# Performance work log

Measured on AMD Instinct MI355X. Metric: run time of the kernel, lower is better.

## Reference

```python
import jax, jax.numpy as jnp
import numpy as np

DIM = 1024
HEADS = 8
DIM_HEAD = 64
HIDDEN = HEADS * DIM_HEAD  # 512
SCALE = DIM_HEAD ** -0.5
BATCH = 16384
EPS = 1e-12  # F.normalize eps


def setup_inputs() -> dict:
    key = jax.random.key(0)
    k0, k1, k2 = jax.random.split(key, 3)
    x = jax.random.normal(k0, (BATCH, DIM), dtype=jnp.float32)
    w_qkv = jax.random.normal(k1, (3 * HIDDEN, DIM), dtype=jnp.float32) * 0.02
    w_out = jax.random.normal(k2, (DIM, HIDDEN), dtype=jnp.float32) * 0.02
    b_out = jnp.zeros((DIM,), dtype=jnp.float32)
    g = jnp.ones((1, DIM), dtype=jnp.float32)
    return {"x": x, "w_qkv": w_qkv, "w_out": w_out, "b_out": b_out, "g": g}


def reference(x, w_qkv, w_out, b_out, g):
    b = x.shape[0]
    # Conv1d(kernel=1, no bias) on n=1 sequence == matmul with (3*hidden, dim) weight
    qkv = x @ w_qkv.T  # (b, 3*hidden)
    q, k, v = jnp.split(qkv, 3, axis=1)  # each (b, hidden)
    # rearrange 'b (h c) n -> b h c n' with n=1 -> (b, h, c)
    q = q.reshape(b, HEADS, DIM_HEAD)
    k = k.reshape(b, HEADS, DIM_HEAD)
    v = v.reshape(b, HEADS, DIM_HEAD)
    # q.softmax(dim=-2) is over the c axis
    q = jax.nn.softmax(q, axis=-1) * SCALE
    # k.softmax(dim=-1) is over the n axis of size 1 -> all ones (kept faithful)
    k = jax.nn.softmax(k[..., None], axis=-1)[..., 0]
    # context = einsum('bhdn,bhen->bhde', k, v); out = einsum('bhde,bhdn->bhen', context, q)
    # with n=1 this collapses to out_e = (sum_d k_d q_d) * v_e; fused to avoid (b,h,d,e)
    s = jnp.einsum('bhd,bhd->bh', k, q)  # (b, h)
    out = s[..., None] * v  # (b, h, e)
    out = out.reshape(b, HIDDEN)  # 'b h c n -> b (h c) n', squeeze(-1)
    # Linear(hidden, dim)
    out = out @ w_out.T + b_out  # (b, dim)
    # RMSNorm_MLP: F.normalize(x, dim=1) * g * sqrt(dim)
    norm = jnp.linalg.norm(out, axis=1, keepdims=True)
    out = out / jnp.maximum(norm, EPS) * g * jnp.sqrt(jnp.float32(DIM))
    return out
```

## Files before the change

kernel.cpp:

```cpp
#include <hip/hip_runtime.h>
#include <hip/hip_bf16.h>


typedef __attribute__((ext_vector_type(8))) short bf16x8;
typedef __attribute__((ext_vector_type(4))) float f32x4;

#define BLK 128
#define BK  32

struct alignas(16) bfvec8 { __hip_bfloat16 h[8]; };

__global__ __launch_bounds__(256)
void cast_bf16(const float* __restrict__ in, bfvec8* __restrict__ out, int n8) {
    int i = blockIdx.x * blockDim.x + threadIdx.x;
    if (i >= n8) return;
    const float4* p = (const float4*)in + (size_t)i * 2;
    float4 a = p[0];
    float4 b = p[1];
    bfvec8 o;
    o.h[0] = __float2bfloat16(a.x); o.h[1] = __float2bfloat16(a.y);
    o.h[2] = __float2bfloat16(a.z); o.h[3] = __float2bfloat16(a.w);
    o.h[4] = __float2bfloat16(b.x); o.h[5] = __float2bfloat16(b.y);
    o.h[6] = __float2bfloat16(b.z); o.h[7] = __float2bfloat16(b.w);
    out[i] = o;
}

template<bool WRITE_BF16>
__global__ __launch_bounds__(256)
void gemm_bt(const __hip_bfloat16* __restrict__ A,
             const __hip_bfloat16* __restrict__ Bt,
             void* __restrict__ Cout,
             const float* __restrict__ bias,
             int M, int N, int K, float alpha)
{
    __shared__ __align__(16) __hip_bfloat16 As[BLK * BK];
    __shared__ __align__(16) __hip_bfloat16 Bs[BLK * BK];

    const int tid  = threadIdx.x;
    const int lane = tid & 63;
    const int wave = tid >> 6;
    const int wm   = wave >> 1;
    const int wn   = wave & 1;
    const int quad = lane >> 4;
    const int tr   = lane & 15;

    const int m0 = blockIdx.y * BLK;
    const int n0 = blockIdx.x * BLK;

    f32x4 acc[4][4];
#pragma unroll
    for (int i = 0; i < 4; ++i)
#pragma unroll
        for (int j = 0; j < 4; ++j)
            acc[i][j] = (f32x4){0.f, 0.f, 0.f, 0.f};

    for (int kt = 0; kt < K; kt += BK) {
#pragma unroll
        for (int i = 0; i < 2; ++i) {
            int L  = i * 256 + wave * 64 + lane;
            int r  = L >> 2;
            int c8 = (L & 3) << 3;
            const __hip_bfloat16* ga = A  + (size_t)(m0 + r) * K + kt + c8;
            const __hip_bfloat16* gb = Bt + (size_t)(n0 + r) * K + kt + c8;
            __builtin_amdgcn_global_load_lds(
                (const __attribute__((address_space(1))) void*)ga,
                (__attribute__((address_space(3))) void*)(As + (size_t)L * 8), 16, 0, 0);
            __builtin_amdgcn_global_load_lds(
                (const __attribute__((address_space(1))) void*)gb,
                (__attribute__((address_space(3))) void*)(Bs + (size_t)L * 8), 16, 0, 0);
        }
        __syncthreads();

        bf16x8 af[4], bf[4];
#pragma unroll
        for (int mi = 0; mi < 4; ++mi)
            af[mi] = *(const bf16x8*)(As + ((wm * 64 + mi * 16 + tr) * BK + quad * 8));
#pragma unroll
        for (int ni = 0; ni < 4; ++ni)
            bf[ni] = *(const bf16x8*)(Bs + ((wn * 64 + ni * 16 + tr) * BK + quad * 8));

#pragma unroll
        for (int mi = 0; mi < 4; ++mi)
#pragma unroll
            for (int ni = 0; ni < 4; ++ni)
                acc[mi][ni] = __builtin_amdgcn_mfma_f32_16x16x32_bf16(
                    af[mi], bf[ni], acc[mi][ni], 0, 0, 0);

        __syncthreads();
    }

#pragma unroll
    for (int mi = 0; mi < 4; ++mi) {
#pragma unroll
        for (int ni = 0; ni < 4; ++ni) {
            const int col = n0 + wn * 64 + ni * 16 + tr;
            float b = 0.f;
            if (!WRITE_BF16 && bias != nullptr) b = bias[col];
#pragma unroll
            for (int r = 0; r < 4; ++r) {
                const int row = m0 + wm * 64 + mi * 16 + quad * 4 + r;
                float val = acc[mi][ni][r] * alpha + b;
                if (WRITE_BF16)
                    ((__hip_bfloat16*)Cout)[(size_t)row * N + col] = __float2bfloat16(val);
                else
                    ((float*)Cout)[(size_t)row * N + col] = val;
            }
        }
    }
}

__global__ __launch_bounds__(256)
void rmsnorm_rows(float* __restrict__ y, const float* __restrict__ g) {
    const int row = blockIdx.x;
    const int tid = threadIdx.x;
    float* p = y + (size_t)row * 1024 + tid * 4;
    float4 v = *(float4*)p;
    float ss = v.x * v.x + v.y * v.y + v.z * v.z + v.w * v.w;
#pragma unroll
    for (int off = 32; off > 0; off >>= 1)
        ss += __shfl_down(ss, off, 64);
    __shared__ float wsum[4];
    if ((tid & 63) == 0) wsum[tid >> 6] = ss;
    __syncthreads();
    const float total = wsum[0] + wsum[1] + wsum[2] + wsum[3];
    const float sc = 32.0f / fmaxf(sqrtf(total), 1e-12f);
    const float4 gv = *(const float4*)(g + tid * 4);
    v.x *= sc * gv.x; v.y *= sc * gv.y; v.z *= sc * gv.z; v.w *= sc * gv.w;
    *(float4*)p = v;
}

extern "C" void kernel_launch(void* const* d_in, const int* in_sizes, int n_in,
                              void* d_out, int out_size, void* d_ws, size_t ws_size,
                              hipStream_t stream) {
    const float* x     = (const float*)d_in[0];
    const float* w_qkv = (const float*)d_in[1];
    const float* w_out = (const float*)d_in[2];
    const float* b_out = (const float*)d_in[3];
    const float* g     = (const float*)d_in[4];

    const int B = 16384, D = 1024, H = 512;

    char* ws = (char*)d_ws;
    __hip_bfloat16* x_bf  = (__hip_bfloat16*)ws;
    __hip_bfloat16* wv_bf = (__hip_bfloat16*)(ws + (size_t)B * D * 2);
    __hip_bfloat16* wo_bf = (__hip_bfloat16*)(ws + (size_t)B * D * 2 + (size_t)H * D * 2);
    __hip_bfloat16* v_bf  = (__hip_bfloat16*)(ws + (size_t)B * D * 2 + (size_t)H * D * 2 * 2);

    cast_bf16<<<(B * D / 8) / 256, 256, 0, stream>>>(x, (bfvec8*)x_bf, B * D / 8);
    cast_bf16<<<(H * D / 8) / 256, 256, 0, stream>>>(w_qkv + (size_t)2 * H * D, (bfvec8*)wv_bf, H * D / 8);
    cast_bf16<<<(D * H / 8) / 256, 256, 0, stream>>>(w_out, (bfvec8*)wo_bf, D * H / 8);

    gemm_bt<true><<<dim3(H / BLK, B / BLK), 256, 0, stream>>>(
        x_bf, wv_bf, (void*)v_bf, nullptr, B, H, D, 0.125f);

    gemm_bt<false><<<dim3(D / BLK, B / BLK), 256, 0, stream>>>(
        v_bf, wo_bf, d_out, b_out, B, D, H, 1.0f);

    rmsnorm_rows<<<B, 256, 0, stream>>>((float*)d_out, g);
}
```

Measured before the change: 213.4 us.

## Fold value and output projections into one precomputed weight matrix

Precomputes a combined weight, W_out·W_v scaled by the constant softmax factor, with a small GEMM on a transposed bf16 copy of W_v. The batch activations then pass through a single 1024x1024 GEMM instead of two chained GEMMs, so the 512-wide intermediate is never written or read. That GEMM now writes bf16 with the bias added, and RMSNorm reads bf16 and writes fp32, which cuts traffic compared with the in-place fp32 pass. Total FLOPs stay about the same, and the code adds a weight-prep GEMM on a small grid plus bf16 rounding of both the fused weight and the pre-norm output.

```diff
diff --git a/kernel.cpp b/kernel.cpp
--- a/kernel.cpp
+++ b/kernel.cpp
@@ -23,6 +23,27 @@
     o.h[4] = __float2bfloat16(b.x); o.h[5] = __float2bfloat16(b.y);
     o.h[6] = __float2bfloat16(b.z); o.h[7] = __float2bfloat16(b.w);
     out[i] = o;
+}
+
+__global__ __launch_bounds__(256)
+void transpose_cast(const float* __restrict__ in, __hip_bfloat16* __restrict__ out,
+                    int rows, int cols) {
+    __shared__ float tile[32][33];
+    const int c = threadIdx.x & 31;
+    const int r8 = threadIdx.x >> 5;
+    const int c0 = blockIdx.x * 32;
+    const int r0 = blockIdx.y * 32;
+#pragma unroll
+    for (int i = 0; i < 4; ++i) {
+        int r = r8 + i * 8;
+        tile[r][c] = in[(size_t)(r0 + r) * cols + c0 + c];
+    }
+    __syncthreads();
+#pragma unroll
+    for (int i = 0; i < 4; ++i) {
+        int r = r8 + i * 8;
+        out[(size_t)(c0 + r) * rows + r0 + c] = __float2bfloat16(tile[c][r]);
+    }
 }
 
 template<bool WRITE_BF16>
@@ -94,8 +115,7 @@
 #pragma unroll
         for (int ni = 0; ni < 4; ++ni) {
             const int col = n0 + wn * 64 + ni * 16 + tr;
-            float b = 0.f;
-            if (!WRITE_BF16 && bias != nullptr) b = bias[col];
+            const float b = (bias != nullptr) ? bias[col] : 0.f;
 #pragma unroll
             for (int r = 0; r < 4; ++r) {
                 const int row = m0 + wm * 64 + mi * 16 + quad * 4 + r;
@@ -110,11 +130,16 @@
 }
 
 __global__ __launch_bounds__(256)
-void rmsnorm_rows(float* __restrict__ y, const float* __restrict__ g) {
+void rmsnorm_rows(const __hip_bfloat16* __restrict__ y, const float* __restrict__ g,
+                  float* __restrict__ out) {
     const int row = blockIdx.x;
     const int tid = threadIdx.x;
-    float* p = y + (size_t)row * 1024 + tid * 4;
-    float4 v = *(float4*)p;
+    const ushort4 u = *(const ushort4*)(y + (size_t)row * 1024 + tid * 4);
+    float4 v;
+    v.x = __bfloat162float(*(const __hip_bfloat16*)&u.x);
+    v.y = __bfloat162float(*(const __hip_bfloat16*)&u.y);
+    v.z = __bfloat162float(*(const __hip_bfloat16*)&u.z);
+    v.w = __bfloat162float(*(const __hip_bfloat16*)&u.w);
     float ss = v.x * v.x + v.y * v.y + v.z * v.z + v.w * v.w;
 #pragma unroll
     for (int off = 32; off > 0; off >>= 1)
@@ -125,8 +150,10 @@
     const float total = wsum[0] + wsum[1] + wsum[2] + wsum[3];
     const float sc = 32.0f / fmaxf(sqrtf(total), 1e-12f);
     const float4 gv = *(const float4*)(g + tid * 4);
-    v.x *= sc * gv.x; v.y *= sc * gv.y; v.z *= sc * gv.z; v.w *= sc * gv.w;
-    *(float4*)p = v;
+    float4 o;
+    o.x = v.x * sc * gv.x; o.y = v.y * sc * gv.y;
+    o.z = v.z * sc * gv.z; o.w = v.w * sc * gv.w;
+    *(float4*)(out + (size_t)row * 1024 + tid * 4) = o;
 }
 
 extern "C" void kernel_launch(void* const* d_in, const int* in_sizes, int n_in,
@@ -139,22 +166,25 @@
     const float* g     = (const float*)d_in[4];
 
     const int B = 16384, D = 1024, H = 512;
+    const float* wv = w_qkv + (size_t)2 * H * D;
 
     char* ws = (char*)d_ws;
-    __hip_bfloat16* x_bf  = (__hip_bfloat16*)ws;
-    __hip_bfloat16* wv_bf = (__hip_bfloat16*)(ws + (size_t)B * D * 2);
-    __hip_bfloat16* wo_bf = (__hip_bfloat16*)(ws + (size_t)B * D * 2 + (size_t)H * D * 2);
-    __hip_bfloat16* v_bf  = (__hip_bfloat16*)(ws + (size_t)B * D * 2 + (size_t)H * D * 2 * 2);
+    size_t off = 0;
+    __hip_bfloat16* x_bf    = (__hip_bfloat16*)(ws + off); off += (size_t)B * D * 2;
+    __hip_bfloat16* wo_bf   = (__hip_bfloat16*)(ws + off); off += (size_t)D * H * 2;
+    __hip_bfloat16* wvT_bf  = (__hip_bfloat16*)(ws + off); off += (size_t)D * H * 2;
+    __hip_bfloat16* weff_bf = (__hip_bfloat16*)(ws + off); off += (size_t)D * D * 2;
+    __hip_bfloat16* y_bf    = (__hip_bfloat16*)(ws + off); off += (size_t)B * D * 2;
 
     cast_bf16<<<(B * D / 8) / 256, 256, 0, stream>>>(x, (bfvec8*)x_bf, B * D / 8);
-    cast_bf16<<<(H * D / 8) / 256, 256, 0, stream>>>(w_qkv + (size_t)2 * H * D, (bfvec8*)wv_bf, H * D / 8);
     cast_bf16<<<(D * H / 8) / 256, 256, 0, stream>>>(w_out, (bfvec8*)wo_bf, D * H / 8);
+    transpose_cast<<<dim3(D / 32, H / 32), 256, 0, stream>>>(wv, wvT_bf, H, D);
 
-    gemm_bt<true><<<dim3(H / BLK, B / BLK), 256, 0, stream>>>(
-        x_bf, wv_bf, (void*)v_bf, nullptr, B, H, D, 0.125f);
+    gemm_bt<true><<<dim3(D / BLK, D / BLK), 256, 0, stream>>>(
+        wo_bf, wvT_bf, (void*)weff_bf, nullptr, D, D, H, 0.125f);
 
-    gemm_bt<false><<<dim3(D / BLK, B / BLK), 256, 0, stream>>>(
-        v_bf, wo_bf, d_out, b_out, B, D, H, 1.0f);
+    gemm_bt<true><<<dim3(D / BLK, B / BLK), 256, 0, stream>>>(
+        x_bf, weff_bf, (void*)y_bf, b_out, B, D, D, 1.0f);
 
-    rmsnorm_rows<<<B, 256, 0, stream>>>((float*)d_out, g);
+    rmsnorm_rows<<<B, 256, 0, stream>>>(y_bf, g, (float*)d_out);
 }
```

Result: slower. 218.4 us (+2.3%).

## Fold Wv and Wout into one effective weight and run a single main GEMM

Applied to the files above, without the earlier changes.

Precomputes Weff = 0.125 * Wout @ Wv (1024x1024) in a small fused kernel, so the two chained GEMMs over the batch become one 16384x1024x1024 GEMM. The main GEMM uses BK=64, an XOR-swizzled LDS layout and an XCD-aware block mapping. It writes bf16 intermediates that a two-rows-per-block RMSNorm kernel reads back. This adds K work in the main GEMM (1024 vs 512 for the second stage) but removes the intermediate V pass and halves intermediate traffic. The extra bf16 rounding of Weff and Y may affect accuracy.

```diff
diff --git a/kernel.cpp b/kernel.cpp
--- a/kernel.cpp
+++ b/kernel.cpp
@@ -5,36 +5,31 @@
 typedef __attribute__((ext_vector_type(8))) short bf16x8;
 typedef __attribute__((ext_vector_type(4))) float f32x4;
 
-#define BLK 128
-#define BK  32
-
 struct alignas(16) bfvec8 { __hip_bfloat16 h[8]; };
 
-__global__ __launch_bounds__(256)
-void cast_bf16(const float* __restrict__ in, bfvec8* __restrict__ out, int n8) {
-    int i = blockIdx.x * blockDim.x + threadIdx.x;
-    if (i >= n8) return;
-    const float4* p = (const float4*)in + (size_t)i * 2;
-    float4 a = p[0];
-    float4 b = p[1];
+__device__ __forceinline__ bfvec8 pack8(float4 a, float4 b) {
     bfvec8 o;
     o.h[0] = __float2bfloat16(a.x); o.h[1] = __float2bfloat16(a.y);
     o.h[2] = __float2bfloat16(a.z); o.h[3] = __float2bfloat16(a.w);
     o.h[4] = __float2bfloat16(b.x); o.h[5] = __float2bfloat16(b.y);
     o.h[6] = __float2bfloat16(b.z); o.h[7] = __float2bfloat16(b.w);
-    out[i] = o;
-}
-
-template<bool WRITE_BF16>
-__global__ __launch_bounds__(256)
-void gemm_bt(const __hip_bfloat16* __restrict__ A,
-             const __hip_bfloat16* __restrict__ Bt,
-             void* __restrict__ Cout,
-             const float* __restrict__ bias,
-             int M, int N, int K, float alpha)
-{
-    __shared__ __align__(16) __hip_bfloat16 As[BLK * BK];
-    __shared__ __align__(16) __hip_bfloat16 Bs[BLK * BK];
+    return o;
+}
+
+__global__ __launch_bounds__(256)
+void cast_bf16(const float* __restrict__ in, bfvec8* __restrict__ out, int n8) {
+    int i = blockIdx.x * blockDim.x + threadIdx.x;
+    if (i >= n8) return;
+    const float4* p = (const float4*)in + (size_t)i * 2;
+    out[i] = pack8(p[0], p[1]);
+}
+
+__global__ __launch_bounds__(256)
+void weff_fused(const float* __restrict__ Wo, const float* __restrict__ Wv,
+                __hip_bfloat16* __restrict__ Weff) {
+    __shared__ __align__(16) __hip_bfloat16 As[128 * 32];
+    __shared__ __align__(16) __hip_bfloat16 Bs[128 * 32];
+    __shared__ __align__(16) float Bf[32 * 132];
 
     const int tid  = threadIdx.x;
     const int lane = tid & 63;
@@ -43,9 +38,8 @@
     const int wn   = wave & 1;
     const int quad = lane >> 4;
     const int tr   = lane & 15;
-
-    const int m0 = blockIdx.y * BLK;
-    const int n0 = blockIdx.x * BLK;
+    const int m0   = blockIdx.y * 128;
+    const int n0   = blockIdx.x * 128;
 
     f32x4 acc[4][4];
 #pragma unroll
@@ -54,14 +48,108 @@
         for (int j = 0; j < 4; ++j)
             acc[i][j] = (f32x4){0.f, 0.f, 0.f, 0.f};
 
-    for (int kt = 0; kt < K; kt += BK) {
+    for (int kt = 0; kt < 512; kt += 32) {
 #pragma unroll
         for (int i = 0; i < 2; ++i) {
-            int L  = i * 256 + wave * 64 + lane;
-            int r  = L >> 2;
-            int c8 = (L & 3) << 3;
-            const __hip_bfloat16* ga = A  + (size_t)(m0 + r) * K + kt + c8;
-            const __hip_bfloat16* gb = Bt + (size_t)(n0 + r) * K + kt + c8;
+            int L = i * 256 + tid;
+            int r = L >> 2, c8 = (L & 3) << 3;
+            const float* s = Wo + (size_t)(m0 + r) * 512 + kt + c8;
+            float4 a = *(const float4*)s, b = *(const float4*)(s + 4);
+            *(bfvec8*)(As + r * 32 + c8) = pack8(a, b);
+        }
+#pragma unroll
+        for (int i = 0; i < 2; ++i) {
+            int L = i * 256 + tid;
+            int kr = L >> 4, c8 = (L & 15) << 3;
+            const float* s = Wv + (size_t)(kt + kr) * 1024 + n0 + c8;
+            float4 a = *(const float4*)s, b = *(const float4*)(s + 4);
+            *(float4*)(Bf + kr * 132 + c8)     = a;
+            *(float4*)(Bf + kr * 132 + c8 + 4) = b;
+        }
+        __syncthreads();
+#pragma unroll
+        for (int i = 0; i < 2; ++i) {
+            int L = i * 256 + tid;
+            int n = L >> 2, k8 = (L & 3) << 3;
+            float4 a, b;
+            a.x = Bf[(k8 + 0) * 132 + n]; a.y = Bf[(k8 + 1) * 132 + n];
+            a.z = Bf[(k8 + 2) * 132 + n]; a.w = Bf[(k8 + 3) * 132 + n];
+            b.x = Bf[(k8 + 4) * 132 + n]; b.y = Bf[(k8 + 5) * 132 + n];
+            b.z = Bf[(k8 + 6) * 132 + n]; b.w = Bf[(k8 + 7) * 132 + n];
+            *(bfvec8*)(Bs + n * 32 + k8) = pack8(a, b);
+        }
+        __syncthreads();
+
+        bf16x8 af[4], bf[4];
+#pragma unroll
+        for (int mi = 0; mi < 4; ++mi)
+            af[mi] = *(const bf16x8*)(As + ((wm * 64 + mi * 16 + tr) * 32 + quad * 8));
+#pragma unroll
+        for (int ni = 0; ni < 4; ++ni)
+            bf[ni] = *(const bf16x8*)(Bs + ((wn * 64 + ni * 16 + tr) * 32 + quad * 8));
+#pragma unroll
+        for (int mi = 0; mi < 4; ++mi)
+#pragma unroll
+            for (int ni = 0; ni < 4; ++ni)
+                acc[mi][ni] = __builtin_amdgcn_mfma_f32_16x16x32_bf16(
+                    af[mi], bf[ni], acc[mi][ni], 0, 0, 0);
+        __syncthreads();
+    }
+
+#pragma unroll
+    for (int mi = 0; mi < 4; ++mi)
+#pragma unroll
+        for (int ni = 0; ni < 4; ++ni) {
+            const int col = n0 + wn * 64 + ni * 16 + tr;
+#pragma unroll
+            for (int r = 0; r < 4; ++r) {
+                const int row = m0 + wm * 64 + mi * 16 + quad * 4 + r;
+                Weff[(size_t)row * 1024 + col] =
+                    __float2bfloat16(acc[mi][ni][r] * 0.125f);
+            }
+        }
+}
+
+__global__ __launch_bounds__(256)
+void main_gemm(const __hip_bfloat16* __restrict__ A,
+               const __hip_bfloat16* __restrict__ Bt,
+               const float* __restrict__ bias,
+               __hip_bfloat16* __restrict__ Y) {
+    __shared__ __align__(16) __hip_bfloat16 As[128 * 64];
+    __shared__ __align__(16) __hip_bfloat16 Bs[128 * 64];
+
+    const int tid  = threadIdx.x;
+    const int lane = tid & 63;
+    const int wave = tid >> 6;
+    const int wm   = wave >> 1;
+    const int wn   = wave & 1;
+    const int quad = lane >> 4;
+    const int tr   = lane & 15;
+
+    const int b   = blockIdx.x;
+    const int xcd = b & 7;
+    const int t   = b >> 3;
+    const int nt  = t & 7;
+    const int mt  = (t >> 3) * 8 + xcd;
+    const int m0  = mt * 128;
+    const int n0  = nt * 128;
+
+    f32x4 acc[4][4];
+#pragma unroll
+    for (int i = 0; i < 4; ++i)
+#pragma unroll
+        for (int j = 0; j < 4; ++j)
+            acc[i][j] = (f32x4){0.f, 0.f, 0.f, 0.f};
+
+    for (int kt = 0; kt < 1024; kt += 64) {
+#pragma unroll
+        for (int i = 0; i < 4; ++i) {
+            int L = i * 256 + tid;
+            int r = L >> 3;
+            int c = L & 7;
+            int kg = (c ^ (r & 7)) << 3;
+            const __hip_bfloat16* ga = A  + (size_t)(m0 + r) * 1024 + kt + kg;
+            const __hip_bfloat16* gb = Bt + (size_t)(n0 + r) * 1024 + kt + kg;
             __builtin_amdgcn_global_load_lds(
                 (const __attribute__((address_space(1))) void*)ga,
                 (__attribute__((address_space(3))) void*)(As + (size_t)L * 8), 16, 0, 0);
@@ -71,62 +159,83 @@
         }
         __syncthreads();
 
-        bf16x8 af[4], bf[4];
-#pragma unroll
-        for (int mi = 0; mi < 4; ++mi)
-            af[mi] = *(const bf16x8*)(As + ((wm * 64 + mi * 16 + tr) * BK + quad * 8));
-#pragma unroll
-        for (int ni = 0; ni < 4; ++ni)
-            bf[ni] = *(const bf16x8*)(Bs + ((wn * 64 + ni * 16 + tr) * BK + quad * 8));
-
-#pragma unroll
-        for (int mi = 0; mi < 4; ++mi)
-#pragma unroll
-            for (int ni = 0; ni < 4; ++ni)
-                acc[mi][ni] = __builtin_amdgcn_mfma_f32_16x16x32_bf16(
-                    af[mi], bf[ni], acc[mi][ni], 0, 0, 0);
-
+#pragma unroll
+        for (int ko = 0; ko < 2; ++ko) {
+            bf16x8 af[4], bf[4];
+#pragma unroll
+            for (int mi = 0; mi < 4; ++mi) {
+                int r = wm * 64 + mi * 16 + tr;
+                int c = (ko * 4 + quad) ^ (r & 7);
+                af[mi] = *(const bf16x8*)(As + (r * 8 + c) * 8);
+            }
+#pragma unroll
+            for (int ni = 0; ni < 4; ++ni) {
+                int r = wn * 64 + ni * 16 + tr;
+                int c = (ko * 4 + quad) ^ (r & 7);
+                bf[ni] = *(const bf16x8*)(Bs + (r * 8 + c) * 8);
+            }
+#pragma unroll
+            for (int mi = 0; mi < 4; ++mi)
+#pragma unroll
+                for (int ni = 0; ni < 4; ++ni)
+                    acc[mi][ni] = __builtin_amdgcn_mfma_f32_16x16x32_bf16(
+                        af[mi], bf[ni], acc[mi][ni], 0, 0, 0);
+        }
         __syncthreads();
     }
 
 #pragma unroll
-    for (int mi = 0; mi < 4; ++mi) {
+    for (int mi = 0; mi < 4; ++mi)
 #pragma unroll
         for (int ni = 0; ni < 4; ++ni) {
             const int col = n0 + wn * 64 + ni * 16 + tr;
-            float b = 0.f;
-            if (!WRITE_BF16 && bias != nullptr) b = bias[col];
+            const float bv = bias[col];
 #pragma unroll
             for (int r = 0; r < 4; ++r) {
                 const int row = m0 + wm * 64 + mi * 16 + quad * 4 + r;
-                float val = acc[mi][ni][r] * alpha + b;
-                if (WRITE_BF16)
-                    ((__hip_bfloat16*)Cout)[(size_t)row * N + col] = __float2bfloat16(val);
-                else
-                    ((float*)Cout)[(size_t)row * N + col] = val;
-            }
-        }
-    }
-}
-
-__global__ __launch_bounds__(256)
-void rmsnorm_rows(float* __restrict__ y, const float* __restrict__ g) {
-    const int row = blockIdx.x;
-    const int tid = threadIdx.x;
-    float* p = y + (size_t)row * 1024 + tid * 4;
-    float4 v = *(float4*)p;
-    float ss = v.x * v.x + v.y * v.y + v.z * v.z + v.w * v.w;
+                Y[(size_t)row * 1024 + col] = __float2bfloat16(acc[mi][ni][r] + bv);
+            }
+        }
+}
+
+__global__ __launch_bounds__(256)
+void rmsnorm2(const __hip_bfloat16* __restrict__ y, const float* __restrict__ g,
+              float* __restrict__ out) {
+    const int wave = threadIdx.x >> 6;
+    const int sub  = wave >> 1;
+    const int t    = threadIdx.x & 127;
+    const int row  = blockIdx.x * 2 + sub;
+    const size_t base = (size_t)row * 1024 + t * 8;
+
+    union { uint4 u; ushort s[8]; } U;
+    U.u = *(const uint4*)(y + base);
+    float v[8];
+#pragma unroll
+    for (int j = 0; j < 8; ++j)
+        v[j] = __bfloat162float(*(const __hip_bfloat16*)&U.s[j]);
+
+    float ss = 0.f;
+#pragma unroll
+    for (int j = 0; j < 8; ++j) ss += v[j] * v[j];
 #pragma unroll
     for (int off = 32; off > 0; off >>= 1)
         ss += __shfl_down(ss, off, 64);
+
     __shared__ float wsum[4];
-    if ((tid & 63) == 0) wsum[tid >> 6] = ss;
+    if ((threadIdx.x & 63) == 0) wsum[wave] = ss;
     __syncthreads();
-    const float total = wsum[0] + wsum[1] + wsum[2] + wsum[3];
+    const float total = wsum[sub * 2] + wsum[sub * 2 + 1];
     const float sc = 32.0f / fmaxf(sqrtf(total), 1e-12f);
-    const float4 gv = *(const float4*)(g + tid * 4);
-    v.x *= sc * gv.x; v.y *= sc * gv.y; v.z *= sc * gv.z; v.w *= sc * gv.w;
-    *(float4*)p = v;
+
+    const float4 g0 = *(const float4*)(g + t * 8);
+    const float4 g1 = *(const float4*)(g + t * 8 + 4);
+    float4 o0, o1;
+    o0.x = v[0] * sc * g0.x; o0.y = v[1] * sc * g0.y;
+    o0.z = v[2] * sc * g0.z; o0.w = v[3] * sc * g0.w;
+    o1.x = v[4] * sc * g1.x; o1.y = v[5] * sc * g1.y;
+    o1.z = v[6] * sc * g1.z; o1.w = v[7] * sc * g1.w;
+    *(float4*)(out + base)     = o0;
+    *(float4*)(out + base + 4) = o1;
 }
 
 extern "C" void kernel_launch(void* const* d_in, const int* in_sizes, int n_in,
@@ -139,22 +248,16 @@
     const float* g     = (const float*)d_in[4];
 
     const int B = 16384, D = 1024, H = 512;
+    const float* wv = w_qkv + (size_t)2 * H * D;
 
     char* ws = (char*)d_ws;
-    __hip_bfloat16* x_bf  = (__hip_bfloat16*)ws;
-    __hip_bfloat16* wv_bf = (__hip_bfloat16*)(ws + (size_t)B * D * 2);
-    __hip_bfloat16* wo_bf = (__hip_bfloat16*)(ws + (size_t)B * D * 2 + (size_t)H * D * 2);
-    __hip_bfloat16* v_bf  = (__hip_bfloat16*)(ws + (size_t)B * D * 2 + (size_t)H * D * 2 * 2);
+    size_t off = 0;
+    __hip_bfloat16* x_bf    = (__hip_bfloat16*)(ws + off); off += (size_t)B * D * 2;
+    __hip_bfloat16* weff_bf = (__hip_bfloat16*)(ws + off); off += (size_t)D * D * 2;
+    __hip_bfloat16* y_bf    = (__hip_bfloat16*)(ws + off); off += (size_t)B * D * 2;
 
     cast_bf16<<<(B * D / 8) / 256, 256, 0, stream>>>(x, (bfvec8*)x_bf, B * D / 8);
-    cast_bf16<<<(H * D / 8) / 256, 256, 0, stream>>>(w_qkv + (size_t)2 * H * D, (bfvec8*)wv_bf, H * D / 8);
-    cast_bf16<<<(D * H / 8) / 256, 256, 0, stream>>>(w_out, (bfvec8*)wo_bf, D * H / 8);
-
-    gemm_bt<true><<<dim3(H / BLK, B / BLK), 256, 0, stream>>>(
-        x_bf, wv_bf, (void*)v_bf, nullptr, B, H, D, 0.125f);
-
-    gemm_bt<false><<<dim3(D / BLK, B / BLK), 256, 0, stream>>>(
-        v_bf, wo_bf, d_out, b_out, B, D, H, 1.0f);
-
-    rmsnorm_rows<<<B, 256, 0, stream>>>((float*)d_out, g);
-}
+    weff_fused<<<dim3(8, 8), 256, 0, stream>>>(w_out, wv, weff_bf);
+    main_gemm<<<1024, 256, 0, stream>>>(x_bf, weff_bf, b_out, y_bf);
+    rmsnorm2<<<B / 2, 256, 0, stream>>>(y_bf, g, (float*)d_out);
+}
```

Result: faster. 203.2 us (-4.8%).
